# Optimization experiments

Measured on AMD Instinct MI355X. Metric: run time of the kernel, lower is better.

The kernel has to match this reference:

```python
import jax, jax.numpy as jnp
import numpy as np

N_EMBD = 1024
N_HEAD = 16
HEAD_DIM = N_EMBD // N_HEAD
EPS = 1e-5


def setup_inputs() -> dict:
    key = jax.random.key(0)
    ks = jax.random.split(key, 6)
    B, S, D = 2, 2048, N_EMBD
    s = 0.02
    return {
        "x": jax.random.normal(ks[0], (B, S, D), jnp.float32),
        "ln1_g": jnp.ones((D,), jnp.float32),
        "ln1_b": jnp.zeros((D,), jnp.float32),
        "w_attn": jax.random.normal(ks[1], (D, 3 * D), jnp.float32) * s,
        "b_attn": jnp.zeros((3 * D,), jnp.float32),
        "w_attn_proj": jax.random.normal(ks[2], (D, D), jnp.float32) * s,
        "b_attn_proj": jnp.zeros((D,), jnp.float32),
        "ln2_g": jnp.ones((D,), jnp.float32),
        "ln2_b": jnp.zeros((D,), jnp.float32),
        "w_fc": jax.random.normal(ks[3], (D, 4 * D), jnp.float32) * s,
        "b_fc": jnp.zeros((4 * D,), jnp.float32),
        "w_fc_proj": jax.random.normal(ks[4], (4 * D, D), jnp.float32) * s,
        "b_fc_proj": jnp.zeros((D,), jnp.float32),
    }


def _layernorm(x, g, b):
    mu = jnp.mean(x, axis=-1, keepdims=True)
    var = jnp.mean(jnp.square(x - mu), axis=-1, keepdims=True)
    return (x - mu) * jax.lax.rsqrt(var + EPS) * g + b


def _block(x, ln1_g, ln1_b, w_attn, b_attn, w_attn_proj, b_attn_proj,
           ln2_g, ln2_b, w_fc, b_fc, w_fc_proj, b_fc_proj):
    B, S, D = x.shape
    h = _layernorm(x, ln1_g, ln1_b)
    qkv = h @ w_attn + b_attn                       # [B,S,3D]
    q, k, v = jnp.split(qkv, 3, axis=-1)
    # [B,H,S,hd]
    q = q.reshape(B, S, N_HEAD, HEAD_DIM).transpose(0, 2, 1, 3)
    k = k.reshape(B, S, N_HEAD, HEAD_DIM).transpose(0, 2, 1, 3)
    v = v.reshape(B, S, N_HEAD, HEAD_DIM).transpose(0, 2, 1, 3)
    scores = jnp.einsum("bhqd,bhkd->bhqk", q, k) / jnp.sqrt(
        jnp.asarray(HEAD_DIM, x.dtype))
    causal = jnp.tril(jnp.ones((S, S), bool))
    scores = jnp.where(causal, scores, -jnp.inf)
    attn = jax.nn.softmax(scores, axis=-1)
    out = jnp.einsum("bhqk,bhkd->bhqd", attn, v)    # [B,H,S,hd]
    out = out.transpose(0, 2, 1, 3).reshape(B, S, D)
    x = x + (out @ w_attn_proj + b_attn_proj)
    h2 = _layernorm(x, ln2_g, ln2_b)
    m = jax.nn.gelu(h2 @ w_fc + b_fc, approximate=False)
    x = x + (m @ w_fc_proj + b_fc_proj)
    return x


def reference(x, ln1_g, ln1_b, w_attn, b_attn, w_attn_proj, b_attn_proj,
              ln2_g, ln2_b, w_fc, b_fc, w_fc_proj, b_fc_proj):
    return _block(x, ln1_g, ln1_b, w_attn, b_attn, w_attn_proj, b_attn_proj,
                  ln2_g, ln2_b, w_fc, b_fc, w_fc_proj, b_fc_proj)
```

## Files before the change

kernel.cpp:

```cpp
#include <hip/hip_runtime.h>
#include <hip/hip_bf16.h>
#include <math.h>

typedef __bf16 bf16_t;
typedef bf16_t bf16x8 __attribute__((ext_vector_type(8)));
typedef float f32x4 __attribute__((ext_vector_type(4)));
typedef unsigned short u16;
typedef u16 ushort8 __attribute__((ext_vector_type(8)));

static __device__ __forceinline__ u16 f2bf(float f) {
    unsigned u = __builtin_bit_cast(unsigned, f);
    u += 0x7FFFu + ((u >> 16) & 1u);
    return (u16)(u >> 16);
}

__global__ __launch_bounds__(256) void ln_kernel(
    const float* __restrict__ x, const float* __restrict__ g,
    const float* __restrict__ be, u16* __restrict__ out)
{
    const int row = blockIdx.x;
    const int tid = threadIdx.x;
    const float4 v = ((const float4*)(x + (long)row * 1024))[tid];
    float s = v.x + v.y + v.z + v.w;
#pragma unroll
    for (int d = 32; d >= 1; d >>= 1) s += __shfl_xor(s, d);
    __shared__ float r1[4], r2[4];
    if ((tid & 63) == 0) r1[tid >> 6] = s;
    __syncthreads();
    const float mean = (r1[0] + r1[1] + r1[2] + r1[3]) * (1.0f / 1024.0f);
    const float dx = v.x - mean, dy = v.y - mean, dz = v.z - mean, dw = v.w - mean;
    float sq = dx * dx + dy * dy + dz * dz + dw * dw;
#pragma unroll
    for (int d = 32; d >= 1; d >>= 1) sq += __shfl_xor(sq, d);
    if ((tid & 63) == 0) r2[tid >> 6] = sq;
    __syncthreads();
    const float var = (r2[0] + r2[1] + r2[2] + r2[3]) * (1.0f / 1024.0f);
    const float rstd = rsqrtf(var + 1e-5f);
    const float4 gg = ((const float4*)g)[tid];
    const float4 bb = ((const float4*)be)[tid];
    ushort4 o;
    o.x = f2bf(dx * rstd * gg.x + bb.x);
    o.y = f2bf(dy * rstd * gg.y + bb.y);
    o.z = f2bf(dz * rstd * gg.z + bb.z);
    o.w = f2bf(dw * rstd * gg.w + bb.w);
    *(ushort4*)&out[(long)row * 1024 + tid * 4] = o;
}

__global__ __launch_bounds__(256) void tcvt_kernel(
    const float* __restrict__ in, u16* __restrict__ outT, int R, int C)
{
    __shared__ float tile[32][33];
    const int tx = threadIdx.x, ty = threadIdx.y;
    const int c0 = blockIdx.x * 32, r0 = blockIdx.y * 32;
#pragma unroll
    for (int i = 0; i < 4; ++i)
        tile[ty + i * 8][tx] = in[(long)(r0 + ty + i * 8) * C + c0 + tx];
    __syncthreads();
#pragma unroll
    for (int i = 0; i < 4; ++i)
        outT[(long)(c0 + ty + i * 8) * R + r0 + tx] = f2bf(tile[tx][ty + i * 8]);
}

template <int BM, int EPI>
static __device__ __forceinline__ void gemm_body(
    const u16* __restrict__ A, const u16* __restrict__ Bt,
    const float* __restrict__ bias, const float* __restrict__ resid,
    void* __restrict__ C, int M, int N, int K)
{
    constexpr int WN = (BM == 128) ? 2 : 4;
    constexpr int MR = 4;
    constexpr int NR = 128 / WN / 16;
    constexpr int AI = BM / 64;
    constexpr int LPW = AI + 2;
    __shared__ __align__(16) u16 As[2][BM * 32];
    __shared__ __align__(16) u16 Bs[2][128 * 32];
    const int tid = threadIdx.x;
    const int lane = tid & 63;
    const int w = tid >> 6;
    const int wm = w / WN, wn = w % WN;
    const int bm = blockIdx.x, bn = blockIdx.y;
    f32x4 acc[MR][NR] = {};

    const u16* Ablk = A + (long)bm * BM * K;
    const u16* Bblk = Bt + (long)bn * 128 * K;
    const int nt = K >> 5;

    auto stage = [&](int buf, int kb) {
#pragma unroll
        for (int i = 0; i < AI; ++i) {
            const int o = (w * AI + i) * 512 + lane * 8;
            const int row = o >> 5, kk = o & 31;
            __builtin_amdgcn_global_load_lds(
                (const __attribute__((address_space(1))) void*)(Ablk + (long)row * K + kb + kk),
                (__attribute__((address_space(3))) void*)(&As[buf][(w * AI + i) * 512]),
                16, 0, 0);
        }
#pragma unroll
        for (int i = 0; i < 2; ++i) {
            const int o = (w * 2 + i) * 512 + lane * 8;
            const int row = o >> 5, kk = o & 31;
            __builtin_amdgcn_global_load_lds(
                (const __attribute__((address_space(1))) void*)(Bblk + (long)row * K + kb + kk),
                (__attribute__((address_space(3))) void*)(&Bs[buf][(w * 2 + i) * 512]),
                16, 0, 0);
        }
    };

    stage(0, 0);
    for (int t = 0; t < nt; ++t) {
        const int cur = t & 1;
        if (t + 1 < nt) {
            stage(cur ^ 1, (t + 1) << 5);
            asm volatile("s_waitcnt vmcnt(%0)" :: "i"(LPW) : "memory");
        } else {
            asm volatile("s_waitcnt vmcnt(0)" ::: "memory");
        }
        __builtin_amdgcn_s_barrier();
        asm volatile("" ::: "memory");

        bf16x8 af[MR], bfr[NR];
#pragma unroll
        for (int m = 0; m < MR; ++m)
            af[m] = *(const bf16x8*)&As[cur][(wm * MR * 16 + m * 16 + (lane & 15)) * 32 + (lane >> 4) * 8];
#pragma unroll
        for (int n = 0; n < NR; ++n)
            bfr[n] = *(const bf16x8*)&Bs[cur][(wn * NR * 16 + n * 16 + (lane & 15)) * 32 + (lane >> 4) * 8];
#pragma unroll
        for (int m = 0; m < MR; ++m)
#pragma unroll
            for (int n = 0; n < NR; ++n)
                acc[m][n] = __builtin_amdgcn_mfma_f32_16x16x32_bf16(af[m], bfr[n], acc[m][n], 0, 0, 0);

        if (t + 1 < nt) {
            asm volatile("" ::: "memory");
            __builtin_amdgcn_s_barrier();
        }
    }

    const int rowBase = bm * BM + wm * MR * 16;
    const int colBase = bn * 128 + wn * NR * 16;
#pragma unroll
    for (int n = 0; n < NR; ++n) {
        const int col = colBase + n * 16 + (lane & 15);
        const float bv = bias[col];
#pragma unroll
        for (int m = 0; m < MR; ++m) {
#pragma unroll
            for (int r = 0; r < 4; ++r) {
                const int row = rowBase + m * 16 + (lane >> 4) * 4 + r;
                float v = acc[m][n][r] + bv;
                if constexpr (EPI == 1) {
                    const float u = v + 0.044715f * v * v * v;
                    v = v / (1.0f + __expf(-1.5957691216057308f * u));
                }
                if constexpr (EPI == 2) {
                    ((float*)C)[(long)row * N + col] = v + resid[(long)row * N + col];
                } else {
                    ((u16*)C)[(long)row * N + col] = f2bf(v);
                }
            }
        }
    }
}

__global__ __launch_bounds__(256) void gemm_qkv(
    const u16* A, const u16* Bt, const float* bias, const float* resid,
    void* C, int M, int N, int K) { gemm_body<128, 0>(A, Bt, bias, resid, C, M, N, K); }
__global__ __launch_bounds__(256) void gemm_fc(
    const u16* A, const u16* Bt, const float* bias, const float* resid,
    void* C, int M, int N, int K) { gemm_body<128, 1>(A, Bt, bias, resid, C, M, N, K); }
__global__ __launch_bounds__(256) void gemm_ap(
    const u16* A, const u16* Bt, const float* bias, const float* resid,
    void* C, int M, int N, int K) { gemm_body<64, 2>(A, Bt, bias, resid, C, M, N, K); }
__global__ __launch_bounds__(256) void gemm_fp(
    const u16* A, const u16* Bt, const float* bias, const float* resid,
    void* C, int M, int N, int K) { gemm_body<64, 2>(A, Bt, bias, resid, C, M, N, K); }

__global__ __launch_bounds__(256) void attn_kernel(
    const u16* __restrict__ qkv, u16* __restrict__ outb)
{
    const int S = 2048;
    const int ipair = blockIdx.x;
    const int bh = blockIdx.y;
    const int b = bh >> 4, h = bh & 15;
    const int tid = threadIdx.x, lane = tid & 63, w = tid >> 6;
    __shared__ __align__(16) u16 Ks[2][64 * 72];
    __shared__ __align__(16) u16 Vs[2][64 * 72];
    __shared__ __align__(16) u16 Ps[4][16 * 72];

    const long base = (long)b * S * 3072;
    const int rstage = tid >> 3;
    const int cg = (tid & 7) * 8;
    const int sw = cg;
    const u16* kbase = qkv + base + 1024 + h * 64 + cg;
    const u16* vbase = qkv + base + 2048 + h * 64 + cg;

    for (int half = 0; half < 2; ++half) {
        const int qt = half ? 31 - ipair : ipair;
        const int q0 = qt * 64;

        bf16x8 qf[2];
        {
            const int qrow = q0 + w * 16 + (lane & 15);
#pragma unroll
            for (int c = 0; c < 2; ++c)
                qf[c] = *(const bf16x8*)&qkv[base + (long)qrow * 3072 + h * 64 + c * 32 + (lane >> 4) * 8];
        }

        f32x4 Of[4] = {};
        float mrow[4], lrow[4];
#pragma unroll
        for (int r = 0; r < 4; ++r) { mrow[r] = -1e30f; lrow[r] = 0.0f; }

        ushort8 kr[2], vr[2];
#pragma unroll
        for (int it = 0; it < 2; ++it) {
            const long ro = (long)(it * 32 + rstage) * 3072;
            kr[it] = *(const ushort8*)&kbase[ro];
            vr[it] = *(const ushort8*)&vbase[ro];
        }
        __syncthreads();
#pragma unroll
        for (int it = 0; it < 2; ++it) {
            const int r = it * 32 + rstage;
            *(ushort8*)&Ks[0][r * 72 + cg] = kr[it];
#pragma unroll
            for (int j = 0; j < 8; ++j)
                Vs[0][(cg + j) * 72 + (r ^ sw)] = vr[it][j];
        }

        for (int kt = 0; kt <= qt; ++kt) {
            const int cur = kt & 1;
            if (kt < qt) {
#pragma unroll
                for (int it = 0; it < 2; ++it) {
                    const long ro = (long)((kt + 1) * 64 + it * 32 + rstage) * 3072;
                    kr[it] = *(const ushort8*)&kbase[ro];
                    vr[it] = *(const ushort8*)&vbase[ro];
                }
            }
            __syncthreads();

            f32x4 Sf[4] = {};
#pragma unroll
            for (int f = 0; f < 4; ++f) {
#pragma unroll
                for (int c = 0; c < 2; ++c) {
                    const bf16x8 kf = *(const bf16x8*)&Ks[cur][(f * 16 + (lane & 15)) * 72 + c * 32 + (lane >> 4) * 8];
                    Sf[f] = __builtin_amdgcn_mfma_f32_16x16x32_bf16(qf[c], kf, Sf[f], 0, 0, 0);
                }
            }
#pragma unroll
            for (int f = 0; f < 4; ++f)
#pragma unroll
                for (int r = 0; r < 4; ++r)
                    Sf[f][r] *= 0.125f;
            if (kt == qt) {
#pragma unroll
                for (int f = 0; f < 4; ++f) {
                    const int kvc = f * 16 + (lane & 15);
#pragma unroll
                    for (int r = 0; r < 4; ++r) {
                        const int qr = w * 16 + (lane >> 4) * 4 + r;
                        if (kvc > qr) Sf[f][r] = -1e30f;
                    }
                }
            }
            float mnew[4], sc[4];
#pragma unroll
            for (int r = 0; r < 4; ++r) {
                float mx = fmaxf(fmaxf(Sf[0][r], Sf[1][r]), fmaxf(Sf[2][r], Sf[3][r]));
#pragma unroll
                for (int d = 1; d < 16; d <<= 1) mx = fmaxf(mx, __shfl_xor(mx, d));
                mnew[r] = fmaxf(mrow[r], mx);
                sc[r] = __expf(mrow[r] - mnew[r]);
                mrow[r] = mnew[r];
            }
#pragma unroll
            for (int f = 0; f < 4; ++f)
#pragma unroll
                for (int r = 0; r < 4; ++r)
                    Sf[f][r] = __expf(Sf[f][r] - mnew[r]);
#pragma unroll
            for (int r = 0; r < 4; ++r) {
                float s = Sf[0][r] + Sf[1][r] + Sf[2][r] + Sf[3][r];
#pragma unroll
                for (int d = 1; d < 16; d <<= 1) s += __shfl_xor(s, d);
                lrow[r] = lrow[r] * sc[r] + s;
            }
#pragma unroll
            for (int f = 0; f < 4; ++f)
#pragma unroll
                for (int r = 0; r < 4; ++r)
                    Of[f][r] *= sc[r];
#pragma unroll
            for (int f = 0; f < 4; ++f)
#pragma unroll
                for (int r = 0; r < 4; ++r)
                    Ps[w][((lane >> 4) * 4 + r) * 72 + f * 16 + (lane & 15)] = f2bf(Sf[f][r]);
#pragma unroll
            for (int f = 0; f < 4; ++f) {
                const int hd = f * 16 + (lane & 15);
#pragma unroll
                for (int c = 0; c < 2; ++c) {
                    const int k0 = c * 32 + (lane >> 4) * 8;
                    const bf16x8 pa = *(const bf16x8*)&Ps[w][(lane & 15) * 72 + k0];
                    const bf16x8 vb = *(const bf16x8*)&Vs[cur][hd * 72 + (k0 ^ (hd & 56))];
                    Of[f] = __builtin_amdgcn_mfma_f32_16x16x32_bf16(pa, vb, Of[f], 0, 0, 0);
                }
            }
            if (kt < qt) {
#pragma unroll
                for (int it = 0; it < 2; ++it) {
                    const int r = it * 32 + rstage;
                    *(ushort8*)&Ks[cur ^ 1][r * 72 + cg] = kr[it];
#pragma unroll
                    for (int j = 0; j < 8; ++j)
                        Vs[cur ^ 1][(cg + j) * 72 + (r ^ sw)] = vr[it][j];
                }
            }
        }

        float inv[4];
#pragma unroll
        for (int r = 0; r < 4; ++r) inv[r] = 1.0f / lrow[r];
#pragma unroll
        for (int f = 0; f < 4; ++f) {
            const int col = h * 64 + f * 16 + (lane & 15);
#pragma unroll
            for (int r = 0; r < 4; ++r) {
                const int qrow = q0 + w * 16 + (lane >> 4) * 4 + r;
                outb[((long)b * S + qrow) * 1024 + col] = f2bf(Of[f][r] * inv[r]);
            }
        }
    }
}

extern "C" void kernel_launch(void* const* d_in, const int* in_sizes, int n_in,
                              void* d_out, int out_size, void* d_ws, size_t ws_size,
                              hipStream_t stream) {
    const float* x      = (const float*)d_in[0];
    const float* ln1_g  = (const float*)d_in[1];
    const float* ln1_b  = (const float*)d_in[2];
    const float* w_attn = (const float*)d_in[3];
    const float* b_attn = (const float*)d_in[4];
    const float* w_ap   = (const float*)d_in[5];
    const float* b_ap   = (const float*)d_in[6];
    const float* ln2_g  = (const float*)d_in[7];
    const float* ln2_b  = (const float*)d_in[8];
    const float* w_fc   = (const float*)d_in[9];
    const float* b_fc   = (const float*)d_in[10];
    const float* w_fp   = (const float*)d_in[11];
    const float* b_fp   = (const float*)d_in[12];
    float* out = (float*)d_out;

    const int R = 4096;
    char* p = (char*)d_ws;
    u16*   wTa  = (u16*)(p);
    u16*   wTap = (u16*)(p + 6291456);
    u16*   wTfc = (u16*)(p + 8388608);
    u16*   wTfp = (u16*)(p + 16777216);
    u16*   hao  = (u16*)(p + 25165824);
    u16*   qkv  = (u16*)(p + 33554432);
    u16*   mb   = hao;
    u16*   h2   = wTa;
    float* x1   = out;

    const dim3 tb(32, 8);
    tcvt_kernel<<<dim3(3072 / 32, 1024 / 32), tb, 0, stream>>>(w_attn, wTa, 1024, 3072);
    tcvt_kernel<<<dim3(1024 / 32, 1024 / 32), tb, 0, stream>>>(w_ap, wTap, 1024, 1024);
    tcvt_kernel<<<dim3(4096 / 32, 1024 / 32), tb, 0, stream>>>(w_fc, wTfc, 1024, 4096);
    tcvt_kernel<<<dim3(1024 / 32, 4096 / 32), tb, 0, stream>>>(w_fp, wTfp, 4096, 1024);

    ln_kernel<<<R, 256, 0, stream>>>(x, ln1_g, ln1_b, hao);
    gemm_qkv<<<dim3(32, 24), 256, 0, stream>>>(hao, wTa, b_attn, nullptr, qkv, R, 3072, 1024);
    attn_kernel<<<dim3(16, 32), 256, 0, stream>>>(qkv, hao);
    gemm_ap<<<dim3(64, 8), 256, 0, stream>>>(hao, wTap, b_ap, x, x1, R, 1024, 1024);
    ln_kernel<<<R, 256, 0, stream>>>(x1, ln2_g, ln2_b, h2);
    gemm_fc<<<dim3(32, 32), 256, 0, stream>>>(h2, wTfc, b_fc, nullptr, mb, R, 4096, 1024);
    gemm_fp<<<dim3(64, 8), 256, 0, stream>>>(mb, wTfp, b_fp, x1, out, R, 1024, 4096);
}
```

Measured before the change: 292.0 us.

## Transpose score MFMA, fold softmax scale into QKV GEMM, lazy rescale

The 1/sqrt(d) scale moves into the QKV GEMM epilogue, where it is applied to the Q columns. The score MFMA operands are swapped so each lane holds one query row across its registers. This replaces the 16-lane shuffle reductions for max and sum with per-lane scalars plus two cross-group shuffles. The running-max rescale of O and l is skipped unless some row's new max exceeds the old one by more than 8, and P is written to LDS as packed 64-bit stores. The deferred rescale lets exponentials reach up to e^8, which risks bf16 precision or overflow on unusual inputs.

```diff
diff --git a/kernel.cpp b/kernel.cpp
--- a/kernel.cpp
+++ b/kernel.cpp
@@ -153,6 +153,9 @@
                     const float u = v + 0.044715f * v * v * v;
                     v = v / (1.0f + __expf(-1.5957691216057308f * u));
                 }
+                if constexpr (EPI == 3) {
+                    if (col < 1024) v *= 0.125f;
+                }
                 if constexpr (EPI == 2) {
                     ((float*)C)[(long)row * N + col] = v + resid[(long)row * N + col];
                 } else {
@@ -165,7 +168,7 @@
 
 __global__ __launch_bounds__(256) void gemm_qkv(
     const u16* A, const u16* Bt, const float* bias, const float* resid,
-    void* C, int M, int N, int K) { gemm_body<128, 0>(A, Bt, bias, resid, C, M, N, K); }
+    void* C, int M, int N, int K) { gemm_body<128, 3>(A, Bt, bias, resid, C, M, N, K); }
 __global__ __launch_bounds__(256) void gemm_fc(
     const u16* A, const u16* Bt, const float* bias, const float* resid,
     void* C, int M, int N, int K) { gemm_body<128, 1>(A, Bt, bias, resid, C, M, N, K); }
@@ -208,9 +211,7 @@
         }
 
         f32x4 Of[4] = {};
-        float mrow[4], lrow[4];
-#pragma unroll
-        for (int r = 0; r < 4; ++r) { mrow[r] = -1e30f; lrow[r] = 0.0f; }
+        float m = -1e30f, l = 0.0f;
 
         ushort8 kr[2], vr[2];
 #pragma unroll
@@ -247,57 +248,59 @@
 #pragma unroll
                 for (int c = 0; c < 2; ++c) {
                     const bf16x8 kf = *(const bf16x8*)&Ks[cur][(f * 16 + (lane & 15)) * 72 + c * 32 + (lane >> 4) * 8];
-                    Sf[f] = __builtin_amdgcn_mfma_f32_16x16x32_bf16(qf[c], kf, Sf[f], 0, 0, 0);
-                }
-            }
+                    Sf[f] = __builtin_amdgcn_mfma_f32_16x16x32_bf16(kf, qf[c], Sf[f], 0, 0, 0);
+                }
+            }
+            if (kt == qt) {
+                const int ql = w * 16 + (lane & 15);
+#pragma unroll
+                for (int f = 0; f < 4; ++f) {
+#pragma unroll
+                    for (int r = 0; r < 4; ++r) {
+                        const int kvl = f * 16 + ((lane >> 4) << 2) + r;
+                        if (kvl > ql) Sf[f][r] = -1e30f;
+                    }
+                }
+            }
+            float pmax = Sf[0][0];
 #pragma unroll
             for (int f = 0; f < 4; ++f)
 #pragma unroll
+                for (int r = 0; r < 4; ++r) pmax = fmaxf(pmax, Sf[f][r]);
+            if (!__all(pmax <= m + 8.0f)) {
+                float pm = pmax;
+                pm = fmaxf(pm, __shfl_xor(pm, 16));
+                pm = fmaxf(pm, __shfl_xor(pm, 32));
+                const float mnew = fmaxf(m, pm);
+                const float sc = __expf(m - mnew);
+                m = mnew;
+                l *= sc;
+                float sco[4];
+#pragma unroll
                 for (int r = 0; r < 4; ++r)
-                    Sf[f][r] *= 0.125f;
-            if (kt == qt) {
-#pragma unroll
-                for (int f = 0; f < 4; ++f) {
-                    const int kvc = f * 16 + (lane & 15);
-#pragma unroll
-                    for (int r = 0; r < 4; ++r) {
-                        const int qr = w * 16 + (lane >> 4) * 4 + r;
-                        if (kvc > qr) Sf[f][r] = -1e30f;
-                    }
-                }
-            }
-            float mnew[4], sc[4];
-#pragma unroll
-            for (int r = 0; r < 4; ++r) {
-                float mx = fmaxf(fmaxf(Sf[0][r], Sf[1][r]), fmaxf(Sf[2][r], Sf[3][r]));
-#pragma unroll
-                for (int d = 1; d < 16; d <<= 1) mx = fmaxf(mx, __shfl_xor(mx, d));
-                mnew[r] = fmaxf(mrow[r], mx);
-                sc[r] = __expf(mrow[r] - mnew[r]);
-                mrow[r] = mnew[r];
-            }
+                    sco[r] = __shfl(sc, ((lane >> 4) << 2) + r);
+#pragma unroll
+                for (int f = 0; f < 4; ++f)
+#pragma unroll
+                    for (int r = 0; r < 4; ++r) Of[f][r] *= sco[r];
+            }
+            float osum = 0.0f;
 #pragma unroll
             for (int f = 0; f < 4; ++f)
 #pragma unroll
-                for (int r = 0; r < 4; ++r)
-                    Sf[f][r] = __expf(Sf[f][r] - mnew[r]);
-#pragma unroll
-            for (int r = 0; r < 4; ++r) {
-                float s = Sf[0][r] + Sf[1][r] + Sf[2][r] + Sf[3][r];
-#pragma unroll
-                for (int d = 1; d < 16; d <<= 1) s += __shfl_xor(s, d);
-                lrow[r] = lrow[r] * sc[r] + s;
-            }
-#pragma unroll
-            for (int f = 0; f < 4; ++f)
-#pragma unroll
-                for (int r = 0; r < 4; ++r)
-                    Of[f][r] *= sc[r];
-#pragma unroll
-            for (int f = 0; f < 4; ++f)
-#pragma unroll
-                for (int r = 0; r < 4; ++r)
-                    Ps[w][((lane >> 4) * 4 + r) * 72 + f * 16 + (lane & 15)] = f2bf(Sf[f][r]);
+                for (int r = 0; r < 4; ++r) {
+                    const float e = __expf(Sf[f][r] - m);
+                    Sf[f][r] = e;
+                    osum += e;
+                }
+            l += osum;
+#pragma unroll
+            for (int f = 0; f < 4; ++f) {
+                const unsigned lo = (unsigned)f2bf(Sf[f][0]) | ((unsigned)f2bf(Sf[f][1]) << 16);
+                const unsigned hi = (unsigned)f2bf(Sf[f][2]) | ((unsigned)f2bf(Sf[f][3]) << 16);
+                uint2 pk; pk.x = lo; pk.y = hi;
+                *(uint2*)&Ps[w][(lane & 15) * 72 + f * 16 + ((lane >> 4) << 2)] = pk;
+            }
 #pragma unroll
             for (int f = 0; f < 4; ++f) {
                 const int hd = f * 16 + (lane & 15);
@@ -321,9 +324,14 @@
             }
         }
 
+        float lt = l;
+        lt += __shfl_xor(lt, 16);
+        lt += __shfl_xor(lt, 32);
+        const float linv = 1.0f / lt;
         float inv[4];
 #pragma unroll
-        for (int r = 0; r < 4; ++r) inv[r] = 1.0f / lrow[r];
+        for (int r = 0; r < 4; ++r)
+            inv[r] = __shfl(linv, ((lane >> 4) << 2) + r);
 #pragma unroll
         for (int f = 0; f < 4; ++f) {
             const int col = h * 64 + f * 16 + (lane & 15);
```

After: 271.5 us. 7.0% less time.
